# Performance work log

Hardware: AMD Instinct MI355X
Metric: run time of the kernel (lower is better)

Reference implementation:

```python
import jax, jax.numpy as jnp
import numpy as np

ALPHA = 0.1
HIDDEN = 512


def setup_inputs() -> dict:
    key = jax.random.key(0)
    k1, k2, k3 = jax.random.split(key, 3)
    input_size = 256
    x = jax.random.normal(k1, (64, 1024, input_size), dtype=jnp.float32)
    W = jax.random.normal(k2, (HIDDEN, HIDDEN), dtype=jnp.float32) / jnp.sqrt(jnp.float32(HIDDEN))
    U = jax.random.normal(k3, (HIDDEN, input_size), dtype=jnp.float32) / jnp.sqrt(jnp.float32(HIDDEN))
    return {"x": x, "W": W, "U": U}


def reference(x, W, U):
    # x: [B, T, I]; recurrence h <- h + alpha * (-h + tanh(h) @ W^T + x_t @ U^T)
    B, T, I = x.shape
    alpha = jnp.float32(ALPHA)
    # precompute input projection for all timesteps: [B, T, H]
    xu = jnp.einsum('bti,hi->bth', x, U)

    def step(h, xu_t):
        dh = -h + jnp.tanh(h) @ W.T + xu_t
        h = h + alpha * dh
        return h, h

    h0 = jnp.zeros((B, W.shape[0]), dtype=x.dtype)
    _, hiddens = jax.lax.scan(step, h0, jnp.swapaxes(xu, 0, 1))  # [T, B, H]
    return jnp.swapaxes(hiddens, 0, 1)  # [B, T, H]
```

## Files before the change

kernel.cpp:

```cpp
#include <hip/hip_runtime.h>

typedef __attribute__((ext_vector_type(4))) float f32x4;
typedef __attribute__((ext_vector_type(8))) short short8;
typedef __attribute__((ext_vector_type(4))) short short4_t;

__device__ __forceinline__ short f2bf(float f) {
  unsigned u = __float_as_uint(f);
  u += 0x7fffu + ((u >> 16) & 1u);
  return (short)(u >> 16);
}

__device__ __forceinline__ float tanh_fast(float x) {
  float e = __expf(2.0f * x);
  return 1.0f - __fdividef(2.0f, e + 1.0f);
}

__global__ __launch_bounds__(256) void convert_wu(
    const float* __restrict__ W, const float* __restrict__ U,
    short* __restrict__ Wb, short* __restrict__ Ub) {
  int i = blockIdx.x * 256 + threadIdx.x;
  if (i < 65536) {
    f32x4 v = ((const f32x4*)W)[i];
    short4_t s;
    s.x = f2bf(v.x); s.y = f2bf(v.y); s.z = f2bf(v.z); s.w = f2bf(v.w);
    ((short4_t*)Wb)[i] = s;
  } else if (i < 98304) {
    int k = i - 65536;
    f32x4 v = ((const f32x4*)U)[k];
    short4_t s;
    s.x = f2bf(v.x); s.y = f2bf(v.y); s.z = f2bf(v.z); s.w = f2bf(v.w);
    ((short4_t*)Ub)[k] = s;
  }
}

__global__ __launch_bounds__(256) void xu_gemm(
    const float* __restrict__ x, const short* __restrict__ Ub,
    float* __restrict__ out) {
  __shared__ __attribute__((aligned(16))) short a_lds[128][272];
  __shared__ __attribute__((aligned(16))) short b_lds[128][272];
  const int tid = threadIdx.x;
  const int mb = blockIdx.x >> 2;
  const int nb = blockIdx.x & 3;

  const float* xb = x + (size_t)mb * (128 * 256);
  for (int c = 0; c < 32; ++c) {
    int idx = c * 256 + tid;
    int r = idx >> 6, c4 = idx & 63;
    f32x4 v = ((const f32x4*)xb)[idx];
    short4_t s;
    s.x = f2bf(v.x); s.y = f2bf(v.y); s.z = f2bf(v.z); s.w = f2bf(v.w);
    *(short4_t*)&a_lds[r][c4 * 4] = s;
  }
  const short* ub = Ub + nb * (128 * 256);
  for (int c = 0; c < 16; ++c) {
    int idx = c * 256 + tid;
    int r = idx >> 5, ch = idx & 31;
    *(short8*)&b_lds[r][ch * 8] = ((const short8*)ub)[idx];
  }
  __syncthreads();

  const int lane = tid & 63, wave = tid >> 6;
  const int wr = wave >> 1, wc = wave & 1;
  const int lr = lane & 15, lk = lane >> 4;
  const f32x4 zero = {0.f, 0.f, 0.f, 0.f};
  f32x4 acc[4][4];
  #pragma unroll
  for (int mt = 0; mt < 4; ++mt)
    #pragma unroll
    for (int nt = 0; nt < 4; ++nt) acc[mt][nt] = zero;

  #pragma unroll
  for (int kt = 0; kt < 8; ++kt) {
    const int k = kt * 32 + lk * 8;
    short8 a[4], b[4];
    #pragma unroll
    for (int mt = 0; mt < 4; ++mt)
      a[mt] = *(const short8*)&a_lds[wr * 64 + mt * 16 + lr][k];
    #pragma unroll
    for (int nt = 0; nt < 4; ++nt)
      b[nt] = *(const short8*)&b_lds[wc * 64 + nt * 16 + lr][k];
    #pragma unroll
    for (int mt = 0; mt < 4; ++mt)
      #pragma unroll
      for (int nt = 0; nt < 4; ++nt)
        acc[mt][nt] = __builtin_amdgcn_mfma_f32_16x16x32_bf16(a[mt], b[nt], acc[mt][nt], 0, 0, 0);
  }

  #pragma unroll
  for (int mt = 0; mt < 4; ++mt)
    #pragma unroll
    for (int nt = 0; nt < 4; ++nt)
      #pragma unroll
      for (int q = 0; q < 4; ++q) {
        int row = mb * 128 + wr * 64 + mt * 16 + lk * 4 + q;
        int col = nb * 128 + wc * 64 + nt * 16 + lr;
        out[(size_t)row * 512 + col] = acc[mt][nt][q];
      }
}

__global__ __launch_bounds__(512, 2) void rnn_scan(
    const short* __restrict__ Wb, float* __restrict__ out) {
  __shared__ __attribute__((aligned(16))) short w_lds[512][136];
  __shared__ __attribute__((aligned(16))) short a_lds[16][520];
  const int tid = threadIdx.x;
  const int blk = blockIdx.x;
  const int lane = tid & 63, wave = tid >> 6;
  const int j0 = wave * 64;
  const int lr = lane & 15, lk = lane >> 4;

  short8 wreg[4][2];
  #pragma unroll
  for (int jt = 0; jt < 4; ++jt) {
    const short* wrow = Wb + (j0 + jt * 16 + lr) * 512 + lk * 8;
    #pragma unroll
    for (int kt = 0; kt < 2; ++kt) {
      wreg[jt][kt] = *(const short8*)(wrow + kt * 32);
      asm volatile("" : "+v"(wreg[jt][kt]));
    }
  }

  const short* pj[4];
  #pragma unroll
  for (int jt = 0; jt < 4; ++jt)
    pj[jt] = Wb + (j0 + jt * 16 + lr) * 512 + lk * 8;

  for (int c = 0; c < 16; ++c) {
    int idx = c * 512 + tid;
    int j = idx >> 4, ch = idx & 15;
    *(short8*)&w_lds[j][ch * 8] = *(const short8*)(Wb + j * 512 + 64 + ch * 8);
  }

  float h[4][4];
  #pragma unroll
  for (int jt = 0; jt < 4; ++jt)
    #pragma unroll
    for (int q = 0; q < 4; ++q) h[jt][q] = 0.f;

  const size_t base = (size_t)(blk * 16 + lk * 4) * 524288 + j0 + lr;
  __syncthreads();

  f32x4 acc[4];
  {
    const float* p = out + base;
    #pragma unroll
    for (int jt = 0; jt < 4; ++jt)
      #pragma unroll
      for (int q = 0; q < 4; ++q)
        acc[jt][q] = p[(size_t)q * 524288 + jt * 16];
  }

  for (int t = 0; t < 1024; ++t) {
    #pragma unroll
    for (int jt = 0; jt < 4; ++jt)
      #pragma unroll
      for (int q = 0; q < 4; ++q)
        a_lds[lk * 4 + q][j0 + jt * 16 + lr] = f2bf(tanh_fast(h[jt][q]));
    __syncthreads();

    short8 s0[4], s1[4];
    #pragma unroll
    for (int jt = 0; jt < 4; ++jt) s0[jt] = *(const short8*)(pj[jt] + 6 * 32);
    #pragma unroll
    for (int jt = 0; jt < 4; ++jt) s1[jt] = *(const short8*)(pj[jt] + 7 * 32);

    #pragma unroll
    for (int kt = 0; kt < 2; ++kt) {
      short8 a8 = *(const short8*)&a_lds[lr][kt * 32 + lk * 8];
      #pragma unroll
      for (int jt = 0; jt < 4; ++jt)
        acc[jt] = __builtin_amdgcn_mfma_f32_16x16x32_bf16(a8, wreg[jt][kt], acc[jt], 0, 0, 0);
    }
    #pragma unroll
    for (int kt = 2; kt < 6; ++kt) {
      short8 a8 = *(const short8*)&a_lds[lr][kt * 32 + lk * 8];
      #pragma unroll
      for (int jt = 0; jt < 4; ++jt) {
        short8 b = *(const short8*)&w_lds[j0 + jt * 16 + lr][(kt - 2) * 32 + lk * 8];
        acc[jt] = __builtin_amdgcn_mfma_f32_16x16x32_bf16(a8, b, acc[jt], 0, 0, 0);
      }
    }
    #pragma unroll
    for (int kt = 6; kt < 16; ++kt) {
      short8 a8 = *(const short8*)&a_lds[lr][kt * 32 + lk * 8];
      if ((kt & 1) == 0) {
        #pragma unroll
        for (int jt = 0; jt < 4; ++jt)
          acc[jt] = __builtin_amdgcn_mfma_f32_16x16x32_bf16(a8, s0[jt], acc[jt], 0, 0, 0);
        if (kt + 2 < 16) {
          #pragma unroll
          for (int jt = 0; jt < 4; ++jt)
            s0[jt] = *(const short8*)(pj[jt] + (kt + 2) * 32);
        }
      } else {
        #pragma unroll
        for (int jt = 0; jt < 4; ++jt)
          acc[jt] = __builtin_amdgcn_mfma_f32_16x16x32_bf16(a8, s1[jt], acc[jt], 0, 0, 0);
        if (kt + 2 < 16) {
          #pragma unroll
          for (int jt = 0; jt < 4; ++jt)
            s1[jt] = *(const short8*)(pj[jt] + (kt + 2) * 32);
        }
      }
    }

    float* po = out + base + (size_t)t * 512;
    #pragma unroll
    for (int jt = 0; jt < 4; ++jt)
      #pragma unroll
      for (int q = 0; q < 4; ++q) {
        float v = 0.9f * h[jt][q] + 0.1f * acc[jt][q];
        h[jt][q] = v;
        po[(size_t)q * 524288 + jt * 16] = v;
      }
    __syncthreads();

    int tn = t + 1; if (tn > 1023) tn = 1023;
    const float* pn = out + base + (size_t)tn * 512;
    #pragma unroll
    for (int jt = 0; jt < 4; ++jt)
      #pragma unroll
      for (int q = 0; q < 4; ++q)
        acc[jt][q] = pn[(size_t)q * 524288 + jt * 16];
  }
}

extern "C" void kernel_launch(void* const* d_in, const int* in_sizes, int n_in,
                              void* d_out, int out_size, void* d_ws, size_t ws_size,
                              hipStream_t stream) {
  (void)in_sizes; (void)n_in; (void)out_size; (void)ws_size;
  const float* x = (const float*)d_in[0];
  const float* W = (const float*)d_in[1];
  const float* U = (const float*)d_in[2];
  float* out = (float*)d_out;
  short* Wb = (short*)d_ws;
  short* Ub = Wb + 512 * 512;

  convert_wu<<<384, 256, 0, stream>>>(W, U, Wb, Ub);
  xu_gemm<<<2048, 256, 0, stream>>>(x, Ub, out);
  rnn_scan<<<4, 512, 0, stream>>>(Wb, out);
}
```

Before: 3.159 ms.

## Pin more W k-slices in AGPRs and interleave LDS and global-streamed MFMA tiles

The recurrent weight W is now split three ways: 3 more k-slices per wave are held permanently in accumulator registers (AGPRs) alongside the existing VGPR slices, the LDS copy shifts to k-slices 5-8, and the remaining slices (9-15) are streamed from global/L2 each step. The MFMA sequence is reordered so the global-streamed slices are interleaved with the LDS slices, giving their loads more latency to hide. The goal is to cut per-step global W traffic and latency on the serial scan's critical path. It raises register pressure, which could cause spills or require AGPR-to-VGPR copies before each MFMA.

```diff
diff --git a/kernel.cpp b/kernel.cpp
--- a/kernel.cpp
+++ b/kernel.cpp
@@ -108,26 +108,32 @@
   const int j0 = wave * 64;
   const int lr = lane & 15, lk = lane >> 4;
 
+  const short* pj[4];
+  #pragma unroll
+  for (int jt = 0; jt < 4; ++jt)
+    pj[jt] = Wb + (j0 + jt * 16 + lr) * 512 + lk * 8;
+
   short8 wreg[4][2];
   #pragma unroll
-  for (int jt = 0; jt < 4; ++jt) {
-    const short* wrow = Wb + (j0 + jt * 16 + lr) * 512 + lk * 8;
+  for (int jt = 0; jt < 4; ++jt)
     #pragma unroll
     for (int kt = 0; kt < 2; ++kt) {
-      wreg[jt][kt] = *(const short8*)(wrow + kt * 32);
+      wreg[jt][kt] = *(const short8*)(pj[jt] + kt * 32);
       asm volatile("" : "+v"(wreg[jt][kt]));
     }
-  }
-
-  const short* pj[4];
-  #pragma unroll
-  for (int jt = 0; jt < 4; ++jt)
-    pj[jt] = Wb + (j0 + jt * 16 + lr) * 512 + lk * 8;
+  short8 wa[4][3];
+  #pragma unroll
+  for (int jt = 0; jt < 4; ++jt)
+    #pragma unroll
+    for (int kt = 0; kt < 3; ++kt) {
+      wa[jt][kt] = *(const short8*)(pj[jt] + (kt + 2) * 32);
+      asm volatile("" : "+a"(wa[jt][kt]));
+    }
 
   for (int c = 0; c < 16; ++c) {
     int idx = c * 512 + tid;
     int j = idx >> 4, ch = idx & 15;
-    *(short8*)&w_lds[j][ch * 8] = *(const short8*)(Wb + j * 512 + 64 + ch * 8);
+    *(short8*)&w_lds[j][ch * 8] = *(const short8*)(Wb + j * 512 + 160 + ch * 8);
   }
 
   float h[4][4];
@@ -159,9 +165,9 @@
 
     short8 s0[4], s1[4];
     #pragma unroll
-    for (int jt = 0; jt < 4; ++jt) s0[jt] = *(const short8*)(pj[jt] + 6 * 32);
-    #pragma unroll
-    for (int jt = 0; jt < 4; ++jt) s1[jt] = *(const short8*)(pj[jt] + 7 * 32);
+    for (int jt = 0; jt < 4; ++jt) s0[jt] = *(const short8*)(pj[jt] + 9 * 32);
+    #pragma unroll
+    for (int jt = 0; jt < 4; ++jt) s1[jt] = *(const short8*)(pj[jt] + 10 * 32);
 
     #pragma unroll
     for (int kt = 0; kt < 2; ++kt) {
@@ -171,36 +177,81 @@
         acc[jt] = __builtin_amdgcn_mfma_f32_16x16x32_bf16(a8, wreg[jt][kt], acc[jt], 0, 0, 0);
     }
     #pragma unroll
-    for (int kt = 2; kt < 6; ++kt) {
+    for (int kt = 0; kt < 3; ++kt) {
+      short8 a8 = *(const short8*)&a_lds[lr][(kt + 2) * 32 + lk * 8];
+      #pragma unroll
+      for (int jt = 0; jt < 4; ++jt)
+        acc[jt] = __builtin_amdgcn_mfma_f32_16x16x32_bf16(a8, wa[jt][kt], acc[jt], 0, 0, 0);
+    }
+    {
+      short8 a8 = *(const short8*)&a_lds[lr][9 * 32 + lk * 8];
+      #pragma unroll
+      for (int jt = 0; jt < 4; ++jt)
+        acc[jt] = __builtin_amdgcn_mfma_f32_16x16x32_bf16(a8, s0[jt], acc[jt], 0, 0, 0);
+      #pragma unroll
+      for (int jt = 0; jt < 4; ++jt) s0[jt] = *(const short8*)(pj[jt] + 11 * 32);
+    }
+    #pragma unroll
+    for (int kt = 5; kt < 7; ++kt) {
       short8 a8 = *(const short8*)&a_lds[lr][kt * 32 + lk * 8];
       #pragma unroll
       for (int jt = 0; jt < 4; ++jt) {
-        short8 b = *(const short8*)&w_lds[j0 + jt * 16 + lr][(kt - 2) * 32 + lk * 8];
+        short8 b = *(const short8*)&w_lds[j0 + jt * 16 + lr][(kt - 5) * 32 + lk * 8];
         acc[jt] = __builtin_amdgcn_mfma_f32_16x16x32_bf16(a8, b, acc[jt], 0, 0, 0);
       }
     }
-    #pragma unroll
-    for (int kt = 6; kt < 16; ++kt) {
+    {
+      short8 a8 = *(const short8*)&a_lds[lr][10 * 32 + lk * 8];
+      #pragma unroll
+      for (int jt = 0; jt < 4; ++jt)
+        acc[jt] = __builtin_amdgcn_mfma_f32_16x16x32_bf16(a8, s1[jt], acc[jt], 0, 0, 0);
+      #pragma unroll
+      for (int jt = 0; jt < 4; ++jt) s1[jt] = *(const short8*)(pj[jt] + 12 * 32);
+    }
+    #pragma unroll
+    for (int kt = 7; kt < 9; ++kt) {
       short8 a8 = *(const short8*)&a_lds[lr][kt * 32 + lk * 8];
-      if ((kt & 1) == 0) {
-        #pragma unroll
-        for (int jt = 0; jt < 4; ++jt)
-          acc[jt] = __builtin_amdgcn_mfma_f32_16x16x32_bf16(a8, s0[jt], acc[jt], 0, 0, 0);
-        if (kt + 2 < 16) {
-          #pragma unroll
-          for (int jt = 0; jt < 4; ++jt)
-            s0[jt] = *(const short8*)(pj[jt] + (kt + 2) * 32);
-        }
-      } else {
-        #pragma unroll
-        for (int jt = 0; jt < 4; ++jt)
-          acc[jt] = __builtin_amdgcn_mfma_f32_16x16x32_bf16(a8, s1[jt], acc[jt], 0, 0, 0);
-        if (kt + 2 < 16) {
-          #pragma unroll
-          for (int jt = 0; jt < 4; ++jt)
-            s1[jt] = *(const short8*)(pj[jt] + (kt + 2) * 32);
-        }
-      }
+      #pragma unroll
+      for (int jt = 0; jt < 4; ++jt) {
+        short8 b = *(const short8*)&w_lds[j0 + jt * 16 + lr][(kt - 5) * 32 + lk * 8];
+        acc[jt] = __builtin_amdgcn_mfma_f32_16x16x32_bf16(a8, b, acc[jt], 0, 0, 0);
+      }
+    }
+    {
+      short8 a8 = *(const short8*)&a_lds[lr][11 * 32 + lk * 8];
+      #pragma unroll
+      for (int jt = 0; jt < 4; ++jt)
+        acc[jt] = __builtin_amdgcn_mfma_f32_16x16x32_bf16(a8, s0[jt], acc[jt], 0, 0, 0);
+      #pragma unroll
+      for (int jt = 0; jt < 4; ++jt) s0[jt] = *(const short8*)(pj[jt] + 13 * 32);
+    }
+    {
+      short8 a8 = *(const short8*)&a_lds[lr][12 * 32 + lk * 8];
+      #pragma unroll
+      for (int jt = 0; jt < 4; ++jt)
+        acc[jt] = __builtin_amdgcn_mfma_f32_16x16x32_bf16(a8, s1[jt], acc[jt], 0, 0, 0);
+      #pragma unroll
+      for (int jt = 0; jt < 4; ++jt) s1[jt] = *(const short8*)(pj[jt] + 14 * 32);
+    }
+    {
+      short8 a8 = *(const short8*)&a_lds[lr][13 * 32 + lk * 8];
+      #pragma unroll
+      for (int jt = 0; jt < 4; ++jt)
+        acc[jt] = __builtin_amdgcn_mfma_f32_16x16x32_bf16(a8, s0[jt], acc[jt], 0, 0, 0);
+      #pragma unroll
+      for (int jt = 0; jt < 4; ++jt) s0[jt] = *(const short8*)(pj[jt] + 15 * 32);
+    }
+    {
+      short8 a8 = *(const short8*)&a_lds[lr][14 * 32 + lk * 8];
+      #pragma unroll
+      for (int jt = 0; jt < 4; ++jt)
+        acc[jt] = __builtin_amdgcn_mfma_f32_16x16x32_bf16(a8, s1[jt], acc[jt], 0, 0, 0);
+    }
+    {
+      short8 a8 = *(const short8*)&a_lds[lr][15 * 32 + lk * 8];
+      #pragma unroll
+      for (int jt = 0; jt < 4; ++jt)
+        acc[jt] = __builtin_amdgcn_mfma_f32_16x16x32_bf16(a8, s0[jt], acc[jt], 0, 0, 0);
     }
 
     float* po = out + base + (size_t)t * 512;
```

After: 3.496 ms. 10.7% more time.
